# Kernel optimization log

Measured on AMD Instinct MI355X. Metric: run time of the kernel, lower is better.

Reference implementation:

```python
import jax, jax.numpy as jnp
import numpy as np

RMS_EPS = 1e-6


def setup_inputs() -> dict:
    key = jax.random.key(0)
    ks = jax.random.split(key, 6)
    B, S, D, F, E = 4, 2048, 1024, 4096, 8
    scale = 0.02
    return {
        "hidden_states": jax.random.normal(ks[0], (B, S, D), dtype=jnp.float32),
        "norm_weight": jnp.ones((D,), dtype=jnp.float32),
        "gate_w": jax.random.normal(ks[1], (E, D), dtype=jnp.float32) * scale,
        "w1": jax.random.normal(ks[2], (E, D, F), dtype=jnp.float32) * scale,
        "w3": jax.random.normal(ks[3], (E, D, F), dtype=jnp.float32) * scale,
        "w2": jax.random.normal(ks[4], (E, F, D), dtype=jnp.float32) * scale,
        "top_k": 2,
    }


def reference(hidden_states, norm_weight, gate_w, w1, w3, w2, top_k):
    B, S, D = hidden_states.shape
    E = gate_w.shape[0]
    # norm_fn: RMSNorm (pre-MoE norm in Mixtral block)
    x = hidden_states * jax.lax.rsqrt(jnp.mean(jnp.square(hidden_states), axis=-1, keepdims=True) + RMS_EPS)
    x = (x * norm_weight).reshape(-1, D)  # [T, D], T = B*S
    # router
    router_logits = jnp.einsum('td,ed->te', x, gate_w)  # [T, E]
    routing = jax.nn.softmax(router_logits.astype(jnp.float32), axis=-1)
    top_w, top_idx = jax.lax.top_k(routing, top_k)  # [T, k]
    top_w = top_w / jnp.sum(top_w, axis=-1, keepdims=True)
    top_w = top_w.astype(x.dtype)
    # dense-masked expert combine: tokens not routed to expert e get weight 0,
    # mathematically identical to the gather/scatter loop in the original.
    out = jnp.zeros_like(x)
    for e in range(E):  # fixed small loop over experts
        w_e = jnp.sum(jnp.where(top_idx == e, top_w, 0.0), axis=-1)  # [T]
        h = jax.nn.silu(x @ w1[e]) * (x @ w3[e])  # [T, F] SwiGLU expert
        out = out + w_e[:, None] * (h @ w2[e])
    return out.reshape(B, S, D), router_logits
```

## Files before the change

kernel.cpp:

```cpp
#include <hip/hip_runtime.h>
#include <hip/hip_bf16.h>

#define T_TOK 8192
#define D_DIM 1024
#define F_DIM 4096
#define E_NUM 8

typedef short s16x8 __attribute__((ext_vector_type(8)));
typedef float f32x4 __attribute__((ext_vector_type(4)));
typedef unsigned short u16x8 __attribute__((ext_vector_type(8)));

__device__ __forceinline__ unsigned short f2bf(float f) {
  union { float f; unsigned int u; } v; v.f = f;
  unsigned int u = v.u;
  return (unsigned short)((u + 0x7FFFu + ((u >> 16) & 1u)) >> 16);
}

__device__ __forceinline__ void async16(const void* g, void* l) {
  __builtin_amdgcn_global_load_lds((const __attribute__((address_space(1))) void*)g,
                                   (__attribute__((address_space(3))) void*)l, 16, 0, 0);
}

__global__ __launch_bounds__(256) void norm_router_kernel(
    const float* __restrict__ hs, const float* __restrict__ nw,
    const float* __restrict__ gw, unsigned short* __restrict__ xb,
    float* __restrict__ logits_out, int* __restrict__ cnt,
    int* __restrict__ ilist, float* __restrict__ wlist) {
  int t = blockIdx.x;
  int tid = threadIdx.x;
  int lane = tid & 63, wid = tid >> 6;
  float4 v = ((const float4*)(hs + (size_t)t * D_DIM))[tid];
  float ss = v.x * v.x + v.y * v.y + v.z * v.z + v.w * v.w;
#pragma unroll
  for (int o = 32; o > 0; o >>= 1) ss += __shfl_xor(ss, o);
  __shared__ float red[4];
  __shared__ float pl[4][8];
  if (lane == 0) red[wid] = ss;
  __syncthreads();
  float ms = (red[0] + red[1] + red[2] + red[3]) * (1.0f / 1024.0f);
  float rs = rsqrtf(ms + 1e-6f);
  float4 wv = ((const float4*)nw)[tid];
  float x0 = v.x * rs * wv.x, x1 = v.y * rs * wv.y;
  float x2 = v.z * rs * wv.z, x3 = v.w * rs * wv.w;
  ((ushort4*)(xb + (size_t)t * D_DIM))[tid] =
      make_ushort4(f2bf(x0), f2bf(x1), f2bf(x2), f2bf(x3));
  float p[8];
#pragma unroll
  for (int e = 0; e < 8; ++e) {
    float4 g = ((const float4*)(gw + (size_t)e * D_DIM))[tid];
    p[e] = x0 * g.x + x1 * g.y + x2 * g.z + x3 * g.w;
  }
#pragma unroll
  for (int e = 0; e < 8; ++e) {
#pragma unroll
    for (int o = 32; o > 0; o >>= 1) p[e] += __shfl_xor(p[e], o);
  }
  if (lane == 0) {
#pragma unroll
    for (int e = 0; e < 8; ++e) pl[wid][e] = p[e];
  }
  __syncthreads();
  if (tid == 0) {
    float l[8];
#pragma unroll
    for (int e = 0; e < 8; ++e) {
      l[e] = pl[0][e] + pl[1][e] + pl[2][e] + pl[3][e];
      logits_out[(size_t)t * 8 + e] = l[e];
    }
    int i0 = 0; float b0 = l[0];
#pragma unroll
    for (int e = 1; e < 8; ++e) if (l[e] > b0) { b0 = l[e]; i0 = e; }
    int i1 = (i0 == 0) ? 1 : 0; float b1 = l[i1];
#pragma unroll
    for (int e = 0; e < 8; ++e) if (e != i0 && l[e] > b1) { b1 = l[e]; i1 = e; }
    float wa = 1.0f / (1.0f + __expf(b1 - b0));
    float wb = 1.0f / (1.0f + __expf(b0 - b1));
    int p0 = atomicAdd(&cnt[i0], 1);
    ilist[i0 * T_TOK + p0] = t * 2;     wlist[i0 * T_TOK + p0] = wa;
    int p1 = atomicAdd(&cnt[i1], 1);
    ilist[i1 * T_TOK + p1] = t * 2 + 1; wlist[i1 * T_TOK + p1] = wb;
  }
}

__global__ __launch_bounds__(256) void transpose_cvt_kernel(
    const float* __restrict__ w1, const float* __restrict__ w3,
    const float* __restrict__ w2, unsigned short* __restrict__ w13t,
    unsigned short* __restrict__ w2t) {
  __shared__ unsigned short tileS[64][72];
  int bx = blockIdx.x;
  int tensor = bx >> 13;
  int e = (bx >> 10) & 7;
  int tl = bx & 1023;
  const float* src; int C, tr, tc;
  if (tensor == 0) {
    src = w1 + (size_t)e * D_DIM * F_DIM; C = F_DIM; tr = tl >> 6; tc = tl & 63;
  } else if (tensor == 1) {
    src = w3 + (size_t)e * D_DIM * F_DIM; C = F_DIM; tr = tl >> 6; tc = tl & 63;
  } else {
    src = w2 + (size_t)e * F_DIM * D_DIM; C = D_DIM; tr = tl >> 4; tc = tl & 15;
  }
  int r0 = tr * 64, c0 = tc * 64;
  int tid = threadIdx.x;
  int rr = tid >> 4, ccb = (tid & 15) * 4;
#pragma unroll
  for (int i = 0; i < 4; ++i) {
    int r = rr + i * 16;
    float4 v = *(const float4*)(src + (size_t)(r0 + r) * C + c0 + ccb);
    tileS[ccb + 0][r] = f2bf(v.x);
    tileS[ccb + 1][r] = f2bf(v.y);
    tileS[ccb + 2][r] = f2bf(v.z);
    tileS[ccb + 3][r] = f2bf(v.w);
  }
  __syncthreads();
  int row = tid >> 2, col = (tid & 3) * 16;
  unsigned short* dp;
  if (tensor < 2) {
    int f = c0 + row;
    int prow = ((f >> 5) * 64) + (f & 31) + (tensor == 1 ? 32 : 0);
    dp = w13t + ((size_t)e * 8192 + prow) * D_DIM + r0 + col;
  } else {
    dp = w2t + ((size_t)e * D_DIM + c0 + row) * F_DIM + r0 + col;
  }
  u16x8 v0, v1;
#pragma unroll
  for (int j = 0; j < 8; ++j) { v0[j] = tileS[row][col + j]; v1[j] = tileS[row][col + 8 + j]; }
  *(u16x8*)dp = v0;
  *(u16x8*)(dp + 8) = v1;
}

__global__ __launch_bounds__(512, 2) void gemm1_kernel(
    const unsigned short* __restrict__ xb, const unsigned short* __restrict__ w13t,
    unsigned short* __restrict__ H, const int* __restrict__ cnt,
    const int* __restrict__ ilist) {
  int flat = blockIdx.x;
  int e = flat & 7;
  int work = flat >> 3;
  int rt = work & 31;
  int ft = work >> 5;
  int ne = cnt[e];
  int r0 = rt * 256;
  if (r0 >= ne) return;
  __shared__ __align__(16) unsigned short As[3 * 8192];
  __shared__ __align__(16) unsigned short Bs[3 * 8192];
  __shared__ int toks[256];
  int tid = threadIdx.x, lane = tid & 63, w = tid >> 6;
  if (tid < 256) toks[tid] = ilist[e * T_TOK + min(r0 + tid, ne - 1)];
  __syncthreads();
  const unsigned short* bpanel = w13t + ((size_t)e * 8192 + ft * 256) * D_DIM;
  int sr0 = tid >> 2, sr1 = sr0 + 128;
  int ch0 = (((tid & 3) ^ ((sr0 >> 1) & 3)) * 8);
  int ch1 = (((tid & 3) ^ ((sr1 >> 1) & 3)) * 8);
  const unsigned short* ap0 = xb + (size_t)(toks[sr0] >> 1) * D_DIM + ch0;
  const unsigned short* ap1 = xb + (size_t)(toks[sr1] >> 1) * D_DIM + ch1;
  const unsigned short* bp0 = bpanel + (size_t)sr0 * D_DIM + ch0;
  const unsigned short* bp1 = bpanel + (size_t)sr1 * D_DIM + ch1;
  int d0 = (sr0 * 32) + (tid & 3) * 8;
  int d1 = d0 + 4096;
  int wr = w >> 2, wc = w & 3;
  int lr = lane & 15, lc = lane >> 4;
  int aoff[8], boff[4];
#pragma unroll
  for (int m = 0; m < 8; ++m) {
    int row = wr * 128 + m * 16 + lr;
    aoff[m] = row * 32 + ((lc ^ ((row >> 1) & 3)) * 8);
  }
#pragma unroll
  for (int n = 0; n < 4; ++n) {
    int row = wc * 64 + n * 16 + lr;
    boff[n] = row * 32 + ((lc ^ ((row >> 1) & 3)) * 8);
  }
  f32x4 acc[8][4] = {};
  async16(ap0, &As[d0]); async16(ap1, &As[d1]);
  async16(bp0, &Bs[d0]); async16(bp1, &Bs[d1]);
  async16(ap0 + 32, &As[8192 + d0]); async16(ap1 + 32, &As[8192 + d1]);
  async16(bp0 + 32, &Bs[8192 + d0]); async16(bp1 + 32, &Bs[8192 + d1]);

#define G1_STEP(T_, BUF_, VMC_, DOST_)                                          \
  {                                                                             \
    asm volatile("s_waitcnt vmcnt(" VMC_ ")" ::: "memory");                     \
    __builtin_amdgcn_s_barrier();                                               \
    const unsigned short* Ab = &As[(BUF_) * 8192];                              \
    const unsigned short* Bb = &Bs[(BUF_) * 8192];                              \
    s16x8 a[8], b[4];                                                           \
    if (DOST_) {                                   \
      int nk = ((T_) + 2) * 32;                                                 \
      async16(ap0 + nk, &As[(((BUF_) + 2) % 3) * 8192 + d0]);                   \
      async16(ap1 + nk, &As[(((BUF_) + 2) % 3) * 8192 + d1]);                   \
    }                                                                           \
    _Pragma("unroll") for (int m = 0; m < 4; ++m)                               \
        a[m] = *(const s16x8*)(Ab + aoff[m]);                                   \
    _Pragma("unroll") for (int n = 0; n < 4; ++n)                               \
        b[n] = *(const s16x8*)(Bb + boff[n]);                                   \
    __builtin_amdgcn_s_setprio(1);                                              \
    _Pragma("unroll") for (int m = 0; m < 4; ++m)                               \
        _Pragma("unroll") for (int n = 0; n < 4; ++n)                           \
            acc[m][n] = __builtin_amdgcn_mfma_f32_16x16x32_bf16(                \
                a[m], b[n], acc[m][n], 0, 0, 0);                                \
    __builtin_amdgcn_s_setprio(0);                                              \
    if (DOST_) {                                   \
      int nk = ((T_) + 2) * 32;                                                 \
      async16(bp0 + nk, &Bs[(((BUF_) + 2) % 3) * 8192 + d0]);                   \
      async16(bp1 + nk, &Bs[(((BUF_) + 2) % 3) * 8192 + d1]);                   \
    }                                                                           \
    _Pragma("unroll") for (int m = 4; m < 8; ++m)                               \
        a[m] = *(const s16x8*)(Ab + aoff[m]);                                   \
    __builtin_amdgcn_s_setprio(1);                                              \
    _Pragma("unroll") for (int m = 4; m < 8; ++m)                               \
        _Pragma("unroll") for (int n = 0; n < 4; ++n)                           \
            acc[m][n] = __builtin_amdgcn_mfma_f32_16x16x32_bf16(                \
                a[m], b[n], acc[m][n], 0, 0, 0);                                \
    __builtin_amdgcn_s_setprio(0);                                              \
  }

  for (int tb = 0; tb < 30; tb += 3) {
    G1_STEP(tb, 0, "4", 1)
    G1_STEP(tb + 1, 1, "4", 1)
    G1_STEP(tb + 2, 2, "4", 1)
  }
  G1_STEP(30, 0, "4", 0)
  G1_STEP(31, 1, "0", 0)
#undef G1_STEP

  int g4 = lane >> 4, cl = lane & 15;
  int fbase = (4 * ft + wc) * 32;
#pragma unroll
  for (int m = 0; m < 8; ++m) {
#pragma unroll
    for (int j = 0; j < 4; ++j) {
      int rloc = wr * 128 + m * 16 + g4 * 4 + j;
      if (r0 + rloc < ne) {
        unsigned short* hp = H + (size_t)toks[rloc] * F_DIM + fbase + cl;
#pragma unroll
        for (int n = 0; n < 2; ++n) {
          float c1 = acc[m][n][j], c3 = acc[m][n + 2][j];
          float h = c1 / (1.0f + __expf(-c1)) * c3;
          hp[n * 16] = f2bf(h);
        }
      }
    }
  }
}

__global__ __launch_bounds__(512, 2) void gemm2_kernel(
    const unsigned short* __restrict__ H, const unsigned short* __restrict__ w2t,
    const int* __restrict__ cnt, const int* __restrict__ ilist,
    const float* __restrict__ wlist, float* __restrict__ out) {
  int flat = blockIdx.x;
  int e = flat & 7;
  int work = flat >> 3;
  int rt = work & 31;
  int nt = work >> 5;
  int ne = cnt[e];
  int r0 = rt * 256;
  if (r0 >= ne) return;
  __shared__ __align__(16) unsigned short As[3 * 8192];
  __shared__ __align__(16) unsigned short Bs[3 * 8192];
  __shared__ int toks[256];
  __shared__ float wts[256];
  int tid = threadIdx.x, lane = tid & 63, w = tid >> 6;
  if (tid < 256) {
    int idx = e * T_TOK + min(r0 + tid, ne - 1);
    toks[tid] = ilist[idx];
    wts[tid] = wlist[idx];
  }
  __syncthreads();
  const unsigned short* bpanel = w2t + ((size_t)e * D_DIM + nt * 256) * F_DIM;
  int sr0 = tid >> 2, sr1 = sr0 + 128;
  int ch0 = (((tid & 3) ^ ((sr0 >> 1) & 3)) * 8);
  int ch1 = (((tid & 3) ^ ((sr1 >> 1) & 3)) * 8);
  const unsigned short* ap0 = H + (size_t)toks[sr0] * F_DIM + ch0;
  const unsigned short* ap1 = H + (size_t)toks[sr1] * F_DIM + ch1;
  const unsigned short* bp0 = bpanel + (size_t)sr0 * F_DIM + ch0;
  const unsigned short* bp1 = bpanel + (size_t)sr1 * F_DIM + ch1;
  int d0 = (sr0 * 32) + (tid & 3) * 8;
  int d1 = d0 + 4096;
  int wr = w >> 2, wc = w & 3;
  int lr = lane & 15, lc = lane >> 4;
  int aoff[8], boff[4];
#pragma unroll
  for (int m = 0; m < 8; ++m) {
    int row = wr * 128 + m * 16 + lr;
    aoff[m] = row * 32 + ((lc ^ ((row >> 1) & 3)) * 8);
  }
#pragma unroll
  for (int n = 0; n < 4; ++n) {
    int row = wc * 64 + n * 16 + lr;
    boff[n] = row * 32 + ((lc ^ ((row >> 1) & 3)) * 8);
  }
  f32x4 acc[8][4] = {};
  async16(ap0, &As[d0]); async16(ap1, &As[d1]);
  async16(bp0, &Bs[d0]); async16(bp1, &Bs[d1]);
  async16(ap0 + 32, &As[8192 + d0]); async16(ap1 + 32, &As[8192 + d1]);
  async16(bp0 + 32, &Bs[8192 + d0]); async16(bp1 + 32, &Bs[8192 + d1]);

#define G2_STEP(T_, BUF_, VMC_, DOST_)                                          \
  {                                                                             \
    asm volatile("s_waitcnt vmcnt(" VMC_ ")" ::: "memory");                     \
    __builtin_amdgcn_s_barrier();                                               \
    const unsigned short* Ab = &As[(BUF_) * 8192];                              \
    const unsigned short* Bb = &Bs[(BUF_) * 8192];                              \
    s16x8 a[8], b[4];                                                           \
    if (DOST_) {                                                                \
      int nk = ((T_) + 2) * 32;                                                 \
      async16(ap0 + nk, &As[(((BUF_) + 2) % 3) * 8192 + d0]);                   \
      async16(ap1 + nk, &As[(((BUF_) + 2) % 3) * 8192 + d1]);                   \
    }                                                                           \
    _Pragma("unroll") for (int m = 0; m < 4; ++m)                               \
        a[m] = *(const s16x8*)(Ab + aoff[m]);                                   \
    _Pragma("unroll") for (int n = 0; n < 4; ++n)                               \
        b[n] = *(const s16x8*)(Bb + boff[n]);                                   \
    __builtin_amdgcn_s_setprio(1);                                              \
    _Pragma("unroll") for (int m = 0; m < 4; ++m)                               \
        _Pragma("unroll") for (int n = 0; n < 4; ++n)                           \
            acc[m][n] = __builtin_amdgcn_mfma_f32_16x16x32_bf16(                \
                a[m], b[n], acc[m][n], 0, 0, 0);                                \
    __builtin_amdgcn_s_setprio(0);                                              \
    if (DOST_) {                                                                \
      int nk = ((T_) + 2) * 32;                                                 \
      async16(bp0 + nk, &Bs[(((BUF_) + 2) % 3) * 8192 + d0]);                   \
      async16(bp1 + nk, &Bs[(((BUF_) + 2) % 3) * 8192 + d1]);                   \
    }                                                                           \
    _Pragma("unroll") for (int m = 4; m < 8; ++m)                               \
        a[m] = *(const s16x8*)(Ab + aoff[m]);                                   \
    __builtin_amdgcn_s_setprio(1);                                              \
    _Pragma("unroll") for (int m = 4; m < 8; ++m)                               \
        _Pragma("unroll") for (int n = 0; n < 4; ++n)                           \
            acc[m][n] = __builtin_amdgcn_mfma_f32_16x16x32_bf16(                \
                a[m], b[n], acc[m][n], 0, 0, 0);                                \
    __builtin_amdgcn_s_setprio(0);                                              \
  }

  for (int tb = 0; tb < 126; tb += 3) {
    G2_STEP(tb, 0, "4", 1)
    G2_STEP(tb + 1, 1, "4", 1)
    G2_STEP(tb + 2, 2, "4", 1)
  }
  G2_STEP(126, 0, "4", 0)
  G2_STEP(127, 1, "0", 0)
#undef G2_STEP

  int g4 = lane >> 4, cl = lane & 15;
#pragma unroll
  for (int m = 0; m < 8; ++m) {
#pragma unroll
    for (int j = 0; j < 4; ++j) {
      int rloc = wr * 128 + m * 16 + g4 * 4 + j;
      if (r0 + rloc < ne) {
        int tok = toks[rloc] >> 1;
        float ww = wts[rloc];
        float* op = out + (size_t)tok * D_DIM + nt * 256 + wc * 64 + cl;
#pragma unroll
        for (int n = 0; n < 4; ++n)
          unsafeAtomicAdd(op + n * 16, ww * acc[m][n][j]);
      }
    }
  }
}

extern "C" void kernel_launch(void* const* d_in, const int* in_sizes, int n_in,
                              void* d_out, int out_size, void* d_ws, size_t ws_size,
                              hipStream_t stream) {
  const float* hs = (const float*)d_in[0];
  const float* nw = (const float*)d_in[1];
  const float* gw = (const float*)d_in[2];
  const float* w1 = (const float*)d_in[3];
  const float* w3 = (const float*)d_in[4];
  const float* w2 = (const float*)d_in[5];
  float* out = (float*)d_out;
  float* logits_out = out + (size_t)T_TOK * D_DIM;

  char* ws = (char*)d_ws;
  unsigned short* xb   = (unsigned short*)(ws);
  unsigned short* w13t = (unsigned short*)(ws + 16777216ull);
  unsigned short* w2t  = (unsigned short*)(ws + 150994944ull);
  unsigned short* H    = (unsigned short*)(ws + 218103808ull);
  int*   ilist = (int*)(ws + 352321536ull);
  float* wlist = (float*)(ws + 352583680ull);
  int*   cnt   = (int*)(ws + 352845824ull);

  hipMemsetAsync(d_out, 0, (size_t)out_size * sizeof(float), stream);
  hipMemsetAsync(cnt, 0, E_NUM * sizeof(int), stream);
  norm_router_kernel<<<T_TOK, 256, 0, stream>>>(hs, nw, gw, xb, logits_out, cnt, ilist, wlist);
  transpose_cvt_kernel<<<3 * E_NUM * 1024, 256, 0, stream>>>(w1, w3, w2, w13t, w2t);
  gemm1_kernel<<<E_NUM * 32 * 32, 512, 0, stream>>>(xb, w13t, H, cnt, ilist);
  gemm2_kernel<<<E_NUM * 32 * 4, 512, 0, stream>>>(H, w2t, cnt, ilist, wlist, out);
}
```

Baseline: 923.6 us.

## Switch GEMMs to double-buffered BK=64 tiles with phased MFMA ping-pong scheduling

```diff
diff --git a/kernel.cpp b/kernel.cpp
--- a/kernel.cpp
+++ b/kernel.cpp
@@ -128,6 +128,73 @@
   *(u16x8*)(dp + 8) = v1;
 }
 
+#define MFMA4(AI_, M_)                                                           \
+  acc[M_][0] = __builtin_amdgcn_mfma_f32_16x16x32_bf16(AI_, b0, acc[M_][0], 0, 0, 0); \
+  acc[M_][1] = __builtin_amdgcn_mfma_f32_16x16x32_bf16(AI_, b1, acc[M_][1], 0, 0, 0); \
+  acc[M_][2] = __builtin_amdgcn_mfma_f32_16x16x32_bf16(AI_, b2, acc[M_][2], 0, 0, 0); \
+  acc[M_][3] = __builtin_amdgcn_mfma_f32_16x16x32_bf16(AI_, b3, acc[M_][3], 0, 0, 0);
+
+#define PHASE_TAIL()                                                             \
+  __builtin_amdgcn_s_barrier();                                                  \
+  asm volatile("s_waitcnt lgkmcnt(0)" ::: "memory");                             \
+  __builtin_amdgcn_sched_barrier(0);                                             \
+  __builtin_amdgcn_s_setprio(1);
+
+#define PHASE_END()                                                              \
+  __builtin_amdgcn_s_setprio(0);                                                 \
+  __builtin_amdgcn_s_barrier();
+
+#define G_ITER(CUR_, NXT_, KT1_, DOST_)                                          \
+  {                                                                              \
+    const unsigned short* Ac = &As[CUR_][0];                                     \
+    const unsigned short* Bc = &Bs[CUR_][0];                                     \
+    s16x8 a0, a1, a2, a3, b0, b1, b2, b3;                                        \
+                                         \
+    a0 = *(const s16x8*)(Ac + aoff[0]); a1 = *(const s16x8*)(Ac + aoff[1]);      \
+    a2 = *(const s16x8*)(Ac + aoff[2]); a3 = *(const s16x8*)(Ac + aoff[3]);      \
+    b0 = *(const s16x8*)(Bc + boff[0]); b1 = *(const s16x8*)(Bc + boff[1]);      \
+    b2 = *(const s16x8*)(Bc + boff[2]); b3 = *(const s16x8*)(Bc + boff[3]);      \
+    if (DOST_) {                                                                 \
+      int ko = (KT1_) * 64;                                                      \
+      async16(ap0 + ko, &As[NXT_][tid * 8]);                                     \
+      async16(ap1 + ko, &As[NXT_][4096 + tid * 8]);                              \
+      async16(ap2 + ko, &As[NXT_][8192 + tid * 8]);                              \
+      async16(ap3 + ko, &As[NXT_][12288 + tid * 8]);                             \
+    }                                                                            \
+    PHASE_TAIL()                                                                 \
+    MFMA4(a0, 0) MFMA4(a1, 1) MFMA4(a2, 2) MFMA4(a3, 3)                          \
+    PHASE_END()                                                                  \
+                                               \
+    a0 = *(const s16x8*)(Ac + aoff[4]); a1 = *(const s16x8*)(Ac + aoff[5]);      \
+    a2 = *(const s16x8*)(Ac + aoff[6]); a3 = *(const s16x8*)(Ac + aoff[7]);      \
+    if (DOST_) {                                                                 \
+      int ko = (KT1_) * 64;                                                      \
+      async16(bp0 + ko, &Bs[NXT_][tid * 8]);                                     \
+      async16(bp1 + ko, &Bs[NXT_][4096 + tid * 8]);                              \
+      async16(bp2 + ko, &Bs[NXT_][8192 + tid * 8]);                              \
+      async16(bp3 + ko, &Bs[NXT_][12288 + tid * 8]);                             \
+    }                                                                            \
+    PHASE_TAIL()                                                                 \
+    MFMA4(a0, 4) MFMA4(a1, 5) MFMA4(a2, 6) MFMA4(a3, 7)                          \
+    PHASE_END()                                                                  \
+                                                       \
+    a0 = *(const s16x8*)(Ac + (aoff[0] ^ 32)); a1 = *(const s16x8*)(Ac + (aoff[1] ^ 32)); \
+    a2 = *(const s16x8*)(Ac + (aoff[2] ^ 32)); a3 = *(const s16x8*)(Ac + (aoff[3] ^ 32)); \
+    b0 = *(const s16x8*)(Bc + (boff[0] ^ 32)); b1 = *(const s16x8*)(Bc + (boff[1] ^ 32)); \
+    b2 = *(const s16x8*)(Bc + (boff[2] ^ 32)); b3 = *(const s16x8*)(Bc + (boff[3] ^ 32)); \
+    PHASE_TAIL()                                                                 \
+    MFMA4(a0, 0) MFMA4(a1, 1) MFMA4(a2, 2) MFMA4(a3, 3)                          \
+    PHASE_END()                                                                  \
+                \
+    a0 = *(const s16x8*)(Ac + (aoff[4] ^ 32)); a1 = *(const s16x8*)(Ac + (aoff[5] ^ 32)); \
+    a2 = *(const s16x8*)(Ac + (aoff[6] ^ 32)); a3 = *(const s16x8*)(Ac + (aoff[7] ^ 32)); \
+    PHASE_TAIL()                                                                 \
+    MFMA4(a0, 4) MFMA4(a1, 5) MFMA4(a2, 6) MFMA4(a3, 7)                          \
+    __builtin_amdgcn_s_setprio(0);                                               \
+    asm volatile("s_waitcnt vmcnt(0)" ::: "memory");                             \
+    __builtin_amdgcn_s_barrier();                                                \
+  }
+
 __global__ __launch_bounds__(512, 2) void gemm1_kernel(
     const unsigned short* __restrict__ xb, const unsigned short* __restrict__ w13t,
     unsigned short* __restrict__ H, const int* __restrict__ cnt,
@@ -140,86 +207,49 @@
   int ne = cnt[e];
   int r0 = rt * 256;
   if (r0 >= ne) return;
-  __shared__ __align__(16) unsigned short As[3 * 8192];
-  __shared__ __align__(16) unsigned short Bs[3 * 8192];
+  __shared__ __align__(16) unsigned short As[2][16384];
+  __shared__ __align__(16) unsigned short Bs[2][16384];
   __shared__ int toks[256];
   int tid = threadIdx.x, lane = tid & 63, w = tid >> 6;
   if (tid < 256) toks[tid] = ilist[e * T_TOK + min(r0 + tid, ne - 1)];
   __syncthreads();
   const unsigned short* bpanel = w13t + ((size_t)e * 8192 + ft * 256) * D_DIM;
-  int sr0 = tid >> 2, sr1 = sr0 + 128;
-  int ch0 = (((tid & 3) ^ ((sr0 >> 1) & 3)) * 8);
-  int ch1 = (((tid & 3) ^ ((sr1 >> 1) & 3)) * 8);
-  const unsigned short* ap0 = xb + (size_t)(toks[sr0] >> 1) * D_DIM + ch0;
-  const unsigned short* ap1 = xb + (size_t)(toks[sr1] >> 1) * D_DIM + ch1;
-  const unsigned short* bp0 = bpanel + (size_t)sr0 * D_DIM + ch0;
-  const unsigned short* bp1 = bpanel + (size_t)sr1 * D_DIM + ch1;
-  int d0 = (sr0 * 32) + (tid & 3) * 8;
-  int d1 = d0 + 4096;
+  int rr = tid >> 3, ch = tid & 7;
+  int coff = ((ch ^ (rr & 7)) * 8);
+  const unsigned short* ap0 = xb + (size_t)(toks[rr] >> 1) * D_DIM + coff;
+  const unsigned short* ap1 = xb + (size_t)(toks[64 + rr] >> 1) * D_DIM + coff;
+  const unsigned short* ap2 = xb + (size_t)(toks[128 + rr] >> 1) * D_DIM + coff;
+  const unsigned short* ap3 = xb + (size_t)(toks[192 + rr] >> 1) * D_DIM + coff;
+  const unsigned short* bp0 = bpanel + (size_t)rr * D_DIM + coff;
+  const unsigned short* bp1 = bpanel + (size_t)(64 + rr) * D_DIM + coff;
+  const unsigned short* bp2 = bpanel + (size_t)(128 + rr) * D_DIM + coff;
+  const unsigned short* bp3 = bpanel + (size_t)(192 + rr) * D_DIM + coff;
   int wr = w >> 2, wc = w & 3;
   int lr = lane & 15, lc = lane >> 4;
   int aoff[8], boff[4];
 #pragma unroll
   for (int m = 0; m < 8; ++m) {
     int row = wr * 128 + m * 16 + lr;
-    aoff[m] = row * 32 + ((lc ^ ((row >> 1) & 3)) * 8);
+    aoff[m] = row * 64 + ((lc ^ (row & 7)) * 8);
   }
 #pragma unroll
   for (int n = 0; n < 4; ++n) {
     int row = wc * 64 + n * 16 + lr;
-    boff[n] = row * 32 + ((lc ^ ((row >> 1) & 3)) * 8);
+    boff[n] = row * 64 + ((lc ^ (row & 7)) * 8);
   }
   f32x4 acc[8][4] = {};
-  async16(ap0, &As[d0]); async16(ap1, &As[d1]);
-  async16(bp0, &Bs[d0]); async16(bp1, &Bs[d1]);
-  async16(ap0 + 32, &As[8192 + d0]); async16(ap1 + 32, &As[8192 + d1]);
-  async16(bp0 + 32, &Bs[8192 + d0]); async16(bp1 + 32, &Bs[8192 + d1]);
-
-#define G1_STEP(T_, BUF_, VMC_, DOST_)                                          \
-  {                                                                             \
-    asm volatile("s_waitcnt vmcnt(" VMC_ ")" ::: "memory");                     \
-    __builtin_amdgcn_s_barrier();                                               \
-    const unsigned short* Ab = &As[(BUF_) * 8192];                              \
-    const unsigned short* Bb = &Bs[(BUF_) * 8192];                              \
-    s16x8 a[8], b[4];                                                           \
-    if (DOST_) {                                   \
-      int nk = ((T_) + 2) * 32;                                                 \
-      async16(ap0 + nk, &As[(((BUF_) + 2) % 3) * 8192 + d0]);                   \
-      async16(ap1 + nk, &As[(((BUF_) + 2) % 3) * 8192 + d1]);                   \
-    }                                                                           \
-    _Pragma("unroll") for (int m = 0; m < 4; ++m)                               \
-        a[m] = *(const s16x8*)(Ab + aoff[m]);                                   \
-    _Pragma("unroll") for (int n = 0; n < 4; ++n)                               \
-        b[n] = *(const s16x8*)(Bb + boff[n]);                                   \
-    __builtin_amdgcn_s_setprio(1);                                              \
-    _Pragma("unroll") for (int m = 0; m < 4; ++m)                               \
-        _Pragma("unroll") for (int n = 0; n < 4; ++n)                           \
-            acc[m][n] = __builtin_amdgcn_mfma_f32_16x16x32_bf16(                \
-                a[m], b[n], acc[m][n], 0, 0, 0);                                \
-    __builtin_amdgcn_s_setprio(0);                                              \
-    if (DOST_) {                                   \
-      int nk = ((T_) + 2) * 32;                                                 \
-      async16(bp0 + nk, &Bs[(((BUF_) + 2) % 3) * 8192 + d0]);                   \
-      async16(bp1 + nk, &Bs[(((BUF_) + 2) % 3) * 8192 + d1]);                   \
-    }                                                                           \
-    _Pragma("unroll") for (int m = 4; m < 8; ++m)                               \
-        a[m] = *(const s16x8*)(Ab + aoff[m]);                                   \
-    __builtin_amdgcn_s_setprio(1);                                              \
-    _Pragma("unroll") for (int m = 4; m < 8; ++m)                               \
-        _Pragma("unroll") for (int n = 0; n < 4; ++n)                           \
-            acc[m][n] = __builtin_amdgcn_mfma_f32_16x16x32_bf16(                \
-                a[m], b[n], acc[m][n], 0, 0, 0);                                \
-    __builtin_amdgcn_s_setprio(0);                                              \
-  }
-
-  for (int tb = 0; tb < 30; tb += 3) {
-    G1_STEP(tb, 0, "4", 1)
-    G1_STEP(tb + 1, 1, "4", 1)
-    G1_STEP(tb + 2, 2, "4", 1)
-  }
-  G1_STEP(30, 0, "4", 0)
-  G1_STEP(31, 1, "0", 0)
-#undef G1_STEP
+  async16(ap0, &As[0][tid * 8]);       async16(ap1, &As[0][4096 + tid * 8]);
+  async16(ap2, &As[0][8192 + tid * 8]); async16(ap3, &As[0][12288 + tid * 8]);
+  async16(bp0, &Bs[0][tid * 8]);       async16(bp1, &Bs[0][4096 + tid * 8]);
+  async16(bp2, &Bs[0][8192 + tid * 8]); async16(bp3, &Bs[0][12288 + tid * 8]);
+  asm volatile("s_waitcnt vmcnt(0)" ::: "memory");
+  __builtin_amdgcn_s_barrier();
+  for (int kt = 0; kt < 14; kt += 2) {
+    G_ITER(0, 1, kt + 1, 1)
+    G_ITER(1, 0, kt + 2, 1)
+  }
+  G_ITER(0, 1, 15, 1)
+  G_ITER(1, 0, 16, 0)
 
   int g4 = lane >> 4, cl = lane & 15;
   int fbase = (4 * ft + wc) * 32;
@@ -253,8 +283,8 @@
   int ne = cnt[e];
   int r0 = rt * 256;
   if (r0 >= ne) return;
-  __shared__ __align__(16) unsigned short As[3 * 8192];
-  __shared__ __align__(16) unsigned short Bs[3 * 8192];
+  __shared__ __align__(16) unsigned short As[2][16384];
+  __shared__ __align__(16) unsigned short Bs[2][16384];
   __shared__ int toks[256];
   __shared__ float wts[256];
   int tid = threadIdx.x, lane = tid & 63, w = tid >> 6;
@@ -265,79 +295,42 @@
   }
   __syncthreads();
   const unsigned short* bpanel = w2t + ((size_t)e * D_DIM + nt * 256) * F_DIM;
-  int sr0 = tid >> 2, sr1 = sr0 + 128;
-  int ch0 = (((tid & 3) ^ ((sr0 >> 1) & 3)) * 8);
-  int ch1 = (((tid & 3) ^ ((sr1 >> 1) & 3)) * 8);
-  const unsigned short* ap0 = H + (size_t)toks[sr0] * F_DIM + ch0;
-  const unsigned short* ap1 = H + (size_t)toks[sr1] * F_DIM + ch1;
-  const unsigned short* bp0 = bpanel + (size_t)sr0 * F_DIM + ch0;
-  const unsigned short* bp1 = bpanel + (size_t)sr1 * F_DIM + ch1;
-  int d0 = (sr0 * 32) + (tid & 3) * 8;
-  int d1 = d0 + 4096;
+  int rr = tid >> 3, ch = tid & 7;
+  int coff = ((ch ^ (rr & 7)) * 8);
+  const unsigned short* ap0 = H + (size_t)toks[rr] * F_DIM + coff;
+  const unsigned short* ap1 = H + (size_t)toks[64 + rr] * F_DIM + coff;
+  const unsigned short* ap2 = H + (size_t)toks[128 + rr] * F_DIM + coff;
+  const unsigned short* ap3 = H + (size_t)toks[192 + rr] * F_DIM + coff;
+  const unsigned short* bp0 = bpanel + (size_t)rr * F_DIM + coff;
+  const unsigned short* bp1 = bpanel + (size_t)(64 + rr) * F_DIM + coff;
+  const unsigned short* bp2 = bpanel + (size_t)(128 + rr) * F_DIM + coff;
+  const unsigned short* bp3 = bpanel + (size_t)(192 + rr) * F_DIM + coff;
   int wr = w >> 2, wc = w & 3;
   int lr = lane & 15, lc = lane >> 4;
   int aoff[8], boff[4];
 #pragma unroll
   for (int m = 0; m < 8; ++m) {
     int row = wr * 128 + m * 16 + lr;
-    aoff[m] = row * 32 + ((lc ^ ((row >> 1) & 3)) * 8);
+    aoff[m] = row * 64 + ((lc ^ (row & 7)) * 8);
   }
 #pragma unroll
   for (int n = 0; n < 4; ++n) {
     int row = wc * 64 + n * 16 + lr;
-    boff[n] = row * 32 + ((lc ^ ((row >> 1) & 3)) * 8);
+    boff[n] = row * 64 + ((lc ^ (row & 7)) * 8);
   }
   f32x4 acc[8][4] = {};
-  async16(ap0, &As[d0]); async16(ap1, &As[d1]);
-  async16(bp0, &Bs[d0]); async16(bp1, &Bs[d1]);
-  async16(ap0 + 32, &As[8192 + d0]); async16(ap1 + 32, &As[8192 + d1]);
-  async16(bp0 + 32, &Bs[8192 + d0]); async16(bp1 + 32, &Bs[8192 + d1]);
-
-#define G2_STEP(T_, BUF_, VMC_, DOST_)                                          \
-  {                                                                             \
-    asm volatile("s_waitcnt vmcnt(" VMC_ ")" ::: "memory");                     \
-    __builtin_amdgcn_s_barrier();                                               \
-    const unsigned short* Ab = &As[(BUF_) * 8192];                              \
-    const unsigned short* Bb = &Bs[(BUF_) * 8192];                              \
-    s16x8 a[8], b[4];                                                           \
-    if (DOST_) {                                                                \
-      int nk = ((T_) + 2) * 32;                                                 \
-      async16(ap0 + nk, &As[(((BUF_) + 2) % 3) * 8192 + d0]);                   \
-      async16(ap1 + nk, &As[(((BUF_) + 2) % 3) * 8192 + d1]);                   \
-    }                                                                           \
-    _Pragma("unroll") for (int m = 0; m < 4; ++m)                               \
-        a[m] = *(const s16x8*)(Ab + aoff[m]);                                   \
-    _Pragma("unroll") for (int n = 0; n < 4; ++n)                               \
-        b[n] = *(const s16x8*)(Bb + boff[n]);                                   \
-    __builtin_amdgcn_s_setprio(1);                                              \
-    _Pragma("unroll") for (int m = 0; m < 4; ++m)                               \
-        _Pragma("unroll") for (int n = 0; n < 4; ++n)                           \
-            acc[m][n] = __builtin_amdgcn_mfma_f32_16x16x32_bf16(                \
-                a[m], b[n], acc[m][n], 0, 0, 0);                                \
-    __builtin_amdgcn_s_setprio(0);                                              \
-    if (DOST_) {                                                                \
-      int nk = ((T_) + 2) * 32;                                                 \
-      async16(bp0 + nk, &Bs[(((BUF_) + 2) % 3) * 8192 + d0]);                   \
-      async16(bp1 + nk, &Bs[(((BUF_) + 2) % 3) * 8192 + d1]);                   \
-    }                                                                           \
-    _Pragma("unroll") for (int m = 4; m < 8; ++m)                               \
-        a[m] = *(const s16x8*)(Ab + aoff[m]);                                   \
-    __builtin_amdgcn_s_setprio(1);                                              \
-    _Pragma("unroll") for (int m = 4; m < 8; ++m)                               \
-        _Pragma("unroll") for (int n = 0; n < 4; ++n)                           \
-            acc[m][n] = __builtin_amdgcn_mfma_f32_16x16x32_bf16(                \
-                a[m], b[n], acc[m][n], 0, 0, 0);                                \
-    __builtin_amdgcn_s_setprio(0);                                              \
-  }
-
-  for (int tb = 0; tb < 126; tb += 3) {
-    G2_STEP(tb, 0, "4", 1)
-    G2_STEP(tb + 1, 1, "4", 1)
-    G2_STEP(tb + 2, 2, "4", 1)
-  }
-  G2_STEP(126, 0, "4", 0)
-  G2_STEP(127, 1, "0", 0)
-#undef G2_STEP
+  async16(ap0, &As[0][tid * 8]);       async16(ap1, &As[0][4096 + tid * 8]);
+  async16(ap2, &As[0][8192 + tid * 8]); async16(ap3, &As[0][12288 + tid * 8]);
+  async16(bp0, &Bs[0][tid * 8]);       async16(bp1, &Bs[0][4096 + tid * 8]);
+  async16(bp2, &Bs[0][8192 + tid * 8]); async16(bp3, &Bs[0][12288 + tid * 8]);
+  asm volatile("s_waitcnt vmcnt(0)" ::: "memory");
+  __builtin_amdgcn_s_barrier();
+  for (int kt = 0; kt < 62; kt += 2) {
+    G_ITER(0, 1, kt + 1, 1)
+    G_ITER(1, 0, kt + 2, 1)
+  }
+  G_ITER(0, 1, 63, 1)
+  G_ITER(1, 0, 64, 0)
 
   int g4 = lane >> 4, cl = lane & 15;
 #pragma unroll
```

After: 1.017 ms. +10.1%, slower.
